# Kernel optimization log

Hardware: AMD Instinct MI355X
Metric: run time of the kernel (lower is better)

Reference implementation:

```python
import math
import jax, jax.numpy as jnp
import numpy as np

CAPACITY_FACTOR = 1.25  # _DEFAULT_EP_CAPACITY_FACTOR
STD = 0.02


def setup_inputs() -> dict:
    key = jax.random.key(0)
    k_x, k_r, k_ug, k_d = jax.random.split(key, 4)
    B, S, D, E, I = 8, 4096, 1024, 16, 2816
    x = jax.random.normal(k_x, (B, S, D), dtype=jnp.float32)
    router = STD * jax.random.truncated_normal(k_r, -3, 3, (D, E)).astype(jnp.float32)
    w_up_gate = STD * jax.random.truncated_normal(k_ug, -3, 3, (E, D, 2 * I)).astype(jnp.float32)
    w_down = STD * jax.random.truncated_normal(k_d, -3, 3, (E, I, D)).astype(jnp.float32)
    return {"x": x, "router": router, "w_up_gate": w_up_gate, "w_down": w_down,
            "num_experts_per_token": 2}


def _routing_stats(selected_experts, router_probs, router_logits, num_experts, k):
    probs = router_probs.astype(jnp.float32)
    logits = router_logits.astype(jnp.float32)
    expert_counts = jnp.sum(jax.nn.one_hot(selected_experts, num_experts, dtype=jnp.float32), axis=(0, 1))
    total = jnp.maximum(jnp.sum(expert_counts), 1.0)
    frac = expert_counts / total
    entropy = -jnp.sum(frac * jnp.log(frac + 1e-06))
    token_fraction = frac * k
    p = jnp.mean(probs, axis=0)
    lb_loss = num_experts * jnp.sum(token_fraction * p)
    z = jax.scipy.special.logsumexp(logits, axis=-1)
    z_loss = jnp.mean(z ** 2)
    return expert_counts, entropy, lb_loss, z_loss


def _moe_forward(x, router, w_up_gate, w_down, k):
    B, S, D = x.shape
    E = router.shape[1]
    T = B * S
    x_flat = x.reshape(T, D)

    router_logits = jnp.einsum('td,de->te', x_flat, router)          # [T,E]
    router_probs = jax.nn.softmax(router_logits, axis=-1)
    topk_logits, selected = jax.lax.top_k(router_logits, k)          # [T,K]
    combine = jax.nn.softmax(topk_logits, axis=-1).astype(x.dtype)   # [T,K]

    stats = _routing_stats(selected, router_probs, router_logits, E, k)

    # ---- capacity-based dispatch ----
    C = int(math.ceil(T * k / E * CAPACITY_FACTOR))                  # static
    TK = T * k
    flat_sel = selected.reshape(TK).astype(jnp.int32)                # token-major priority
    oh = jax.nn.one_hot(flat_sel, E, dtype=jnp.int32)                # [TK,E]
    pos = jnp.take_along_axis(jnp.cumsum(oh, axis=0), flat_sel[:, None], axis=1)[:, 0] - 1
    keep = pos < C                                                   # [TK]
    pos_safe = jnp.where(keep, pos, 0)
    token_idx = jnp.arange(TK, dtype=jnp.int32) // k

    vals = jnp.where(keep[:, None], x_flat[token_idx], 0.0)          # [TK,D]
    expert_in = jnp.zeros((E, C, D), dtype=x.dtype).at[flat_sel, pos_safe].add(vals)

    # ---- grouped SwiGLU MLP ----
    h = jnp.einsum('ecd,edf->ecf', expert_in, w_up_gate)             # [E,C,2I]
    I = w_down.shape[1]
    gate, up = h[..., :I], h[..., I:]
    act = jax.nn.silu(gate) * up                                     # [E,C,I]
    expert_out = jnp.einsum('eci,eid->ecd', act, w_down)             # [E,C,D]

    # ---- combine ----
    gathered = expert_out[flat_sel, pos_safe]                        # [TK,D]
    w = (combine.reshape(TK) * keep.astype(x.dtype))[:, None]
    routed = (gathered * w).reshape(T, k, D).sum(axis=1)             # [T,D]
    return routed.reshape(B, S, D), stats


def reference(x, router, w_up_gate, w_down, num_experts_per_token):
    routed, (counts, entropy, lb_loss, z_loss) = _moe_forward(
        x, router, w_up_gate, w_down, num_experts_per_token)
    return routed, counts, entropy, lb_loss, z_loss
```

## Files before the change

kernel.cpp:

```cpp
#include <hip/hip_runtime.h>
#include <math.h>

#define T_TOK 32768
#define TKA   65536
#define DIM   1024
#define NE    16
#define IDIM  2816
#define CAP   5120

typedef short short8 __attribute__((ext_vector_type(8)));
typedef float floatx4 __attribute__((ext_vector_type(4)));

__device__ __forceinline__ unsigned short f2bf(float f) {
  unsigned int u = __float_as_uint(f);
  u = u + 0x7FFFu + ((u >> 16) & 1u);
  return (unsigned short)(u >> 16);
}
__device__ __forceinline__ float bf2f(unsigned short h) {
  return __uint_as_float(((unsigned int)h) << 16);
}

__device__ __forceinline__ void gld_lds16(const void* g, void* l) {
  __builtin_amdgcn_global_load_lds(
      (const __attribute__((address_space(1))) unsigned int*)(unsigned long long)g,
      (__attribute__((address_space(3))) unsigned int*)(unsigned int)(unsigned long long)l,
      16, 0, 0);
}


__global__ void cvtx_kernel(const float* __restrict__ in, unsigned short* __restrict__ out) {
  size_t i = ((size_t)blockIdx.x * 256 + threadIdx.x) * 8;
  float4 a = *(const float4*)(in + i);
  float4 b = *(const float4*)(in + i + 4);
  short8 v;
  v[0] = (short)f2bf(a.x); v[1] = (short)f2bf(a.y); v[2] = (short)f2bf(a.z); v[3] = (short)f2bf(a.w);
  v[4] = (short)f2bf(b.x); v[5] = (short)f2bf(b.y); v[6] = (short)f2bf(b.z); v[7] = (short)f2bf(b.w);
  *(short8*)(out + i) = v;
}

__global__ void transpose_cvt(const float* __restrict__ in, unsigned short* __restrict__ out,
                              int R, int Cin) {
  int e = blockIdx.z;
  size_t base = (size_t)e * R * Cin;
  int ct = blockIdx.x;
  int rt = blockIdx.y;
  __shared__ unsigned short Ts[64][72];
  int tx = threadIdx.x & 63, ty = threadIdx.x >> 6;
#pragma unroll
  for (int j = 0; j < 16; j++) {
    int r = rt * 64 + ty + j * 4;
    int c = ct * 64 + tx;
    Ts[tx][ty + j * 4] = f2bf(in[base + (size_t)r * Cin + c]);
  }
  __syncthreads();
#pragma unroll
  for (int j = 0; j < 16; j++) {
    int cl = ty + j * 4;
    out[base + (size_t)(ct * 64 + cl) * R + rt * 64 + tx] = Ts[cl][tx];
  }
}


__global__ void router_kernel(const float* __restrict__ x, const float* __restrict__ router,
                              float* __restrict__ logits) {
  int tid = blockIdx.x * 256 + threadIdx.x;
  int tk = tid >> 4, e = tid & 15;
  const float* xr = x + (size_t)tk * DIM;
  float acc = 0.f;
#pragma unroll 8
  for (int d = 0; d < DIM; d++) acc = fmaf(xr[d], router[d * NE + e], acc);
  logits[tid] = acc;
}

__global__ void topk_kernel(const float* __restrict__ logits, int* __restrict__ sel,
                            float* __restrict__ wcomb, float* __restrict__ prob_sums,
                            int* __restrict__ counts_raw, float* __restrict__ z2sum) {
  __shared__ float ps[16];
  __shared__ int   cs[16];
  __shared__ float zs;
  int tid = threadIdx.x;
  if (tid < 16) { ps[tid] = 0.f; cs[tid] = 0; }
  if (tid == 0) zs = 0.f;
  __syncthreads();
  int t = blockIdx.x * 256 + tid;
  float l[16];
#pragma unroll
  for (int e = 0; e < 16; e++) l[e] = logits[(size_t)t * 16 + e];
  float m1 = l[0]; int e1 = 0;
#pragma unroll
  for (int e = 1; e < 16; e++) if (l[e] > m1) { m1 = l[e]; e1 = e; }
  float m2 = -3.4e38f; int e2 = 0;
#pragma unroll
  for (int e = 0; e < 16; e++) if (e != e1 && l[e] > m2) { m2 = l[e]; e2 = e; }
  float b  = __expf(m2 - m1);
  float w1 = 1.f / (1.f + b);
  sel[t * 2] = e1; sel[t * 2 + 1] = e2;
  wcomb[t * 2] = w1; wcomb[t * 2 + 1] = 1.f - w1;
  float s = 0.f;
  float pexp[16];
#pragma unroll
  for (int e = 0; e < 16; e++) { pexp[e] = __expf(l[e] - m1); s += pexp[e]; }
  float inv = 1.f / s;
#pragma unroll
  for (int e = 0; e < 16; e++) atomicAdd(&ps[e], pexp[e] * inv);
  atomicAdd(&cs[e1], 1); atomicAdd(&cs[e2], 1);
  float z = m1 + __logf(s);
  atomicAdd(&zs, z * z);
  __syncthreads();
  if (tid < 16) { atomicAdd(&prob_sums[tid], ps[tid]); atomicAdd(&counts_raw[tid], cs[tid]); }
  if (tid == 0) atomicAdd(z2sum, zs);
}

__global__ void hist_kernel(const int* __restrict__ sel, int* __restrict__ bhist) {
  __shared__ int h[16];
  int tid = threadIdx.x;
  if (tid < 16) h[tid] = 0;
  __syncthreads();
  atomicAdd(&h[sel[blockIdx.x * 256 + tid]], 1);
  __syncthreads();
  if (tid < 16) bhist[blockIdx.x * 16 + tid] = h[tid];
}

__global__ void scan_kernel(const int* __restrict__ bhist, int* __restrict__ bbase,
                            int* __restrict__ capc) {
  int e = threadIdx.x;
  if (e >= 16) return;
  int run = 0;
  for (int b = 0; b < 256; b++) { bbase[b * 16 + e] = run; run += bhist[b * 16 + e]; }
  capc[e] = run < CAP ? run : CAP;
}

__global__ void rank_kernel(const int* __restrict__ sel, const int* __restrict__ bbase,
                            int* __restrict__ pos_tk, int* __restrict__ scat) {
  __shared__ int se[256];
  int i = threadIdx.x;
  int a = blockIdx.x * 256 + i;
  int e = sel[a];
  se[i] = e;
  __syncthreads();
  int r = 0;
  for (int j = 0; j < i; j++) r += (se[j] == e) ? 1 : 0;
  int pos = bbase[blockIdx.x * 16 + e] + r;
  if (pos < CAP) { pos_tk[a] = pos; scat[e * CAP + pos] = a >> 1; }
  else           { pos_tk[a] = -1; }
}


__global__ __launch_bounds__(256) void gemm1_kernel(
    const unsigned short* __restrict__ xb, const unsigned short* __restrict__ wtg,
    const int* __restrict__ scat, const int* __restrict__ capc,
    const unsigned short* __restrict__ zrow, unsigned short* __restrict__ act) {
  int e = blockIdx.z, ct = blockIdx.x, it = blockIdx.y;
  if (ct * 128 >= capc[e]) return;
  __shared__ __align__(16) unsigned short As[128 * 64];
  __shared__ __align__(16) unsigned short Bg[64 * 64];
  __shared__ __align__(16) unsigned short Bu[64 * 64];
  const int t = threadIdx.x, w = t >> 6, l = t & 63;
  const int lr8   = l >> 3;
  const int koffs = ((l & 7) ^ lr8) * 8;

  const unsigned short* aptr[4];
#pragma unroll
  for (int j = 0; j < 4; j++) {
    int c0 = ct * 128 + w * 32 + j * 8 + lr8;
    int tok = scat[e * CAP + c0];
    aptr[j] = (tok >= 0 ? xb + (size_t)tok * DIM : zrow) + koffs;
  }
  const unsigned short* bgp[2];
  const unsigned short* bup[2];
#pragma unroll
  for (int j = 0; j < 2; j++) {
    int n0 = it * 64 + w * 16 + j * 8 + lr8;
    bgp[j] = wtg + ((size_t)e * (2 * IDIM) + n0) * DIM + koffs;
    bup[j] = bgp[j] + (size_t)IDIM * DIM;
  }

  floatx4 accg[8], accu[8];
#pragma unroll
  for (int i = 0; i < 8; i++) {
    accg[i] = (floatx4){0.f, 0.f, 0.f, 0.f};
    accu[i] = (floatx4){0.f, 0.f, 0.f, 0.f};
  }
  const int wm = w >> 1, wn = w & 1;
  const int rl = l & 15, lq = l >> 4, sx = l & 7;

  for (int k0 = 0; k0 < DIM; k0 += 64) {
    __syncthreads();
#pragma unroll
    for (int j = 0; j < 4; j++)
      gld_lds16(aptr[j] + k0, (char*)As + w * 4096 + j * 1024);
#pragma unroll
    for (int j = 0; j < 2; j++) {
      gld_lds16(bgp[j] + k0, (char*)Bg + w * 2048 + j * 1024);
      gld_lds16(bup[j] + k0, (char*)Bu + w * 2048 + j * 1024);
    }
    __syncthreads();
#pragma unroll
    for (int ks = 0; ks < 2; ks++) {
      const int slot = ((ks * 4 + lq) ^ sx) * 8;
      short8 af[4], bgf[2], buf2[2];
#pragma unroll
      for (int mi = 0; mi < 4; mi++)
        af[mi] = *(const short8*)(As + (wm * 64 + mi * 16 + rl) * 64 + slot);
#pragma unroll
      for (int ni = 0; ni < 2; ni++) {
        bgf[ni]  = *(const short8*)(Bg + (wn * 32 + ni * 16 + rl) * 64 + slot);
        buf2[ni] = *(const short8*)(Bu + (wn * 32 + ni * 16 + rl) * 64 + slot);
      }
#pragma unroll
      for (int mi = 0; mi < 4; mi++)
#pragma unroll
        for (int ni = 0; ni < 2; ni++) {
          accg[mi * 2 + ni] = __builtin_amdgcn_mfma_f32_16x16x32_bf16(af[mi], bgf[ni],  accg[mi * 2 + ni], 0, 0, 0);
          accu[mi * 2 + ni] = __builtin_amdgcn_mfma_f32_16x16x32_bf16(af[mi], buf2[ni], accu[mi * 2 + ni], 0, 0, 0);
        }
    }
  }

  size_t abase = ((size_t)e * CAP + (size_t)ct * 128) * IDIM + (size_t)it * 64;
#pragma unroll
  for (int mi = 0; mi < 4; mi++)
#pragma unroll
    for (int reg = 0; reg < 4; reg++) {
      int m = wm * 64 + mi * 16 + lq * 4 + reg;
#pragma unroll
      for (int ni = 0; ni < 2; ni++) {
        int n = wn * 32 + ni * 16 + (l & 15);
        float g = accg[mi * 2 + ni][reg];
        float u = accu[mi * 2 + ni][reg];
        float a = g / (1.f + __expf(-g)) * u;
        act[abase + (size_t)m * IDIM + n] = f2bf(a);
      }
    }
}


__global__ __launch_bounds__(256) void gemm2_kernel(
    const unsigned short* __restrict__ act, const unsigned short* __restrict__ wtd,
    const int* __restrict__ capc, unsigned short* __restrict__ eout) {
  int e = blockIdx.z, ct = blockIdx.x, it = blockIdx.y;
  if (ct * 128 >= capc[e]) return;
  __shared__ __align__(16) unsigned short As[128 * 64];
  __shared__ __align__(16) unsigned short Bs[64 * 64];
  const int t = threadIdx.x, w = t >> 6, l = t & 63;
  const int lr8   = l >> 3;
  const int koffs = ((l & 7) ^ lr8) * 8;

  const unsigned short* aptr[4];
#pragma unroll
  for (int j = 0; j < 4; j++)
    aptr[j] = act + ((size_t)e * CAP + ct * 128 + w * 32 + j * 8 + lr8) * IDIM + koffs;
  const unsigned short* bptr[2];
#pragma unroll
  for (int j = 0; j < 2; j++)
    bptr[j] = wtd + ((size_t)e * DIM + it * 64 + w * 16 + j * 8 + lr8) * IDIM + koffs;

  floatx4 acc[8];
#pragma unroll
  for (int i = 0; i < 8; i++) acc[i] = (floatx4){0.f, 0.f, 0.f, 0.f};
  const int wm = w >> 1, wn = w & 1;
  const int rl = l & 15, lq = l >> 4, sx = l & 7;

  for (int k0 = 0; k0 < IDIM; k0 += 64) {
    __syncthreads();
#pragma unroll
    for (int j = 0; j < 4; j++)
      gld_lds16(aptr[j] + k0, (char*)As + w * 4096 + j * 1024);
#pragma unroll
    for (int j = 0; j < 2; j++)
      gld_lds16(bptr[j] + k0, (char*)Bs + w * 2048 + j * 1024);
    __syncthreads();
#pragma unroll
    for (int ks = 0; ks < 2; ks++) {
      const int slot = ((ks * 4 + lq) ^ sx) * 8;
      short8 af[4], bf2[2];
#pragma unroll
      for (int mi = 0; mi < 4; mi++)
        af[mi] = *(const short8*)(As + (wm * 64 + mi * 16 + rl) * 64 + slot);
#pragma unroll
      for (int ni = 0; ni < 2; ni++)
        bf2[ni] = *(const short8*)(Bs + (wn * 32 + ni * 16 + rl) * 64 + slot);
#pragma unroll
      for (int mi = 0; mi < 4; mi++)
#pragma unroll
        for (int ni = 0; ni < 2; ni++)
          acc[mi * 2 + ni] = __builtin_amdgcn_mfma_f32_16x16x32_bf16(af[mi], bf2[ni], acc[mi * 2 + ni], 0, 0, 0);
    }
  }

  size_t obase = ((size_t)e * CAP + (size_t)ct * 128) * DIM + (size_t)it * 64;
#pragma unroll
  for (int mi = 0; mi < 4; mi++)
#pragma unroll
    for (int reg = 0; reg < 4; reg++) {
      int m = wm * 64 + mi * 16 + lq * 4 + reg;
#pragma unroll
      for (int ni = 0; ni < 2; ni++) {
        int n = wn * 32 + ni * 16 + (l & 15);
        eout[obase + (size_t)m * DIM + n] = f2bf(acc[mi * 2 + ni][reg]);
      }
    }
}


__global__ void combine_kernel(const unsigned short* __restrict__ eout,
                               const int* __restrict__ sel, const int* __restrict__ pos_tk,
                               const float* __restrict__ wcomb, float* __restrict__ routed) {
  int tok = blockIdx.x;
  int d = threadIdx.x * 4;
  float a0 = 0.f, a1 = 0.f, a2 = 0.f, a3 = 0.f;
#pragma unroll
  for (int s = 0; s < 2; s++) {
    int a = tok * 2 + s;
    int p = pos_tk[a];
    if (p >= 0) {
      int e = sel[a];
      float wgt = wcomb[a];
      const unsigned short* row = eout + ((size_t)e * CAP + p) * DIM + d;
      ushort4 r = *(const ushort4*)row;
      a0 += wgt * bf2f(r.x); a1 += wgt * bf2f(r.y);
      a2 += wgt * bf2f(r.z); a3 += wgt * bf2f(r.w);
    }
  }
  float4 o = {a0, a1, a2, a3};
  *(float4*)(routed + (size_t)tok * DIM + d) = o;
}

__global__ void finalize_kernel(const int* __restrict__ counts_raw, const float* __restrict__ psums,
                                const float* __restrict__ z2sum, float* __restrict__ tail) {
  if (threadIdx.x != 0 || blockIdx.x != 0) return;
  float ent = 0.f, lb = 0.f;
  for (int e = 0; e < 16; e++) {
    float c = (float)counts_raw[e];
    tail[e] = c;
    float frac = c / 65536.f;
    ent -= frac * logf(frac + 1e-6f);
    lb += frac * 2.f * (psums[e] / 32768.f);
  }
  tail[16] = ent;
  tail[17] = 16.f * lb;
  tail[18] = z2sum[0] / 32768.f;
}


extern "C" void kernel_launch(void* const* d_in, const int* in_sizes, int n_in,
                              void* d_out, int out_size, void* d_ws, size_t ws_size,
                              hipStream_t stream) {
  (void)in_sizes; (void)n_in; (void)out_size; (void)ws_size;
  const float* x         = (const float*)d_in[0];
  const float* router    = (const float*)d_in[1];
  const float* w_up_gate = (const float*)d_in[2];
  const float* w_down    = (const float*)d_in[3];
  float* out = (float*)d_out;

  char* p = (char*)d_ws;
  size_t off = 0;
  auto alc = [&](size_t n) { void* r = p + off; off += (n + 255) & ~(size_t)255; return r; };

  unsigned short* xb   = (unsigned short*)alc((size_t)T_TOK * DIM * 2);
  unsigned short* wtg  = (unsigned short*)alc((size_t)NE * 2 * IDIM * DIM * 2);
  unsigned short* wtd  = (unsigned short*)alc((size_t)NE * DIM * IDIM * 2);
  unsigned short* act  = (unsigned short*)alc((size_t)NE * CAP * IDIM * 2);
  unsigned short* eout = (unsigned short*)alc((size_t)NE * CAP * DIM * 2);
  float* logits = (float*)alc((size_t)T_TOK * NE * 4);
  int*   sel    = (int*)alc((size_t)TKA * 4);
  float* wcomb  = (float*)alc((size_t)TKA * 4);
  int*   pos_tk = (int*)alc((size_t)TKA * 4);
  int*   scat   = (int*)alc((size_t)NE * CAP * 4);
  int*   bhist  = (int*)alc(256 * 16 * 4);
  int*   bbase  = (int*)alc(256 * 16 * 4);
  int*   capc   = (int*)alc(64);
  int*   counts_raw = (int*)alc(64);
  float* psums  = (float*)alc(64);
  float* z2     = (float*)alc(64);
  unsigned short* zrow = (unsigned short*)alc(DIM * 2);

  hipMemsetAsync(counts_raw, 0, 64, stream);
  hipMemsetAsync(psums, 0, 64, stream);
  hipMemsetAsync(z2, 0, 64, stream);
  hipMemsetAsync(scat, 0xFF, (size_t)NE * CAP * 4, stream);
  hipMemsetAsync(zrow, 0, DIM * 2, stream);

  cvtx_kernel<<<T_TOK * DIM / (256 * 8), 256, 0, stream>>>(x, xb);
  transpose_cvt<<<dim3(2 * IDIM / 64, DIM / 64, NE), 256, 0, stream>>>(w_up_gate, wtg, DIM, 2 * IDIM);
  transpose_cvt<<<dim3(DIM / 64, IDIM / 64, NE), 256, 0, stream>>>(w_down, wtd, IDIM, DIM);

  router_kernel<<<T_TOK * NE / 256, 256, 0, stream>>>(x, router, logits);
  topk_kernel<<<T_TOK / 256, 256, 0, stream>>>(logits, sel, wcomb, psums, counts_raw, z2);
  hist_kernel<<<TKA / 256, 256, 0, stream>>>(sel, bhist);
  scan_kernel<<<1, 64, 0, stream>>>(bhist, bbase, capc);
  rank_kernel<<<TKA / 256, 256, 0, stream>>>(sel, bbase, pos_tk, scat);

  gemm1_kernel<<<dim3(CAP / 128, IDIM / 64, NE), 256, 0, stream>>>(xb, wtg, scat, capc, zrow, act);
  gemm2_kernel<<<dim3(CAP / 128, DIM / 64, NE), 256, 0, stream>>>(act, wtd, capc, eout);

  combine_kernel<<<T_TOK, 256, 0, stream>>>(eout, sel, pos_tk, wcomb, out);
  finalize_kernel<<<1, 64, 0, stream>>>(counts_raw, psums, z2, out + (size_t)T_TOK * DIM);
}
```

Measured before the change: 2.482 ms.

## Double-buffer LDS tiles in both expert GEMMs and stage scan input in LDS

Both grouped GEMM kernels now keep two LDS buffers for the A and B tiles. Each iteration issues the asynchronous global-to-LDS loads for the next K slice before running the MFMAs on the current one, and uses one barrier per stage instead of two. The goal is to hide global load latency behind matrix math. In exchange, LDS use per block doubles (about 64KB for gemm1 and 48KB for gemm2), which can cut the number of resident blocks per CU. The scan kernel also copies the block histogram into shared memory with all 256 threads before the 16-thread serial prefix scan.

```diff
diff --git a/kernel.cpp b/kernel.cpp
--- a/kernel.cpp
+++ b/kernel.cpp
@@ -123,11 +123,16 @@
 
 __global__ void scan_kernel(const int* __restrict__ bhist, int* __restrict__ bbase,
                             int* __restrict__ capc) {
-  int e = threadIdx.x;
-  if (e >= 16) return;
-  int run = 0;
-  for (int b = 0; b < 256; b++) { bbase[b * 16 + e] = run; run += bhist[b * 16 + e]; }
-  capc[e] = run < CAP ? run : CAP;
+  __shared__ int h[256 * 16];
+  int t = threadIdx.x;
+  for (int i = t; i < 256 * 16 / 4; i += 256)
+    ((int4*)h)[i] = ((const int4*)bhist)[i];
+  __syncthreads();
+  if (t < 16) {
+    int run = 0;
+    for (int b = 0; b < 256; b++) { bbase[b * 16 + t] = run; run += h[b * 16 + t]; }
+    capc[t] = run < CAP ? run : CAP;
+  }
 }
 
 __global__ void rank_kernel(const int* __restrict__ sel, const int* __restrict__ bbase,
@@ -152,9 +157,9 @@
     const unsigned short* __restrict__ zrow, unsigned short* __restrict__ act) {
   int e = blockIdx.z, ct = blockIdx.x, it = blockIdx.y;
   if (ct * 128 >= capc[e]) return;
-  __shared__ __align__(16) unsigned short As[128 * 64];
-  __shared__ __align__(16) unsigned short Bg[64 * 64];
-  __shared__ __align__(16) unsigned short Bu[64 * 64];
+  __shared__ __align__(16) unsigned short As0[128 * 64], As1[128 * 64];
+  __shared__ __align__(16) unsigned short Bg0[64 * 64],  Bg1[64 * 64];
+  __shared__ __align__(16) unsigned short Bu0[64 * 64],  Bu1[64 * 64];
   const int t = threadIdx.x, w = t >> 6, l = t & 63;
   const int lr8   = l >> 3;
   const int koffs = ((l & 7) ^ lr8) * 8;
@@ -184,8 +189,7 @@
   const int wm = w >> 1, wn = w & 1;
   const int rl = l & 15, lq = l >> 4, sx = l & 7;
 
-  for (int k0 = 0; k0 < DIM; k0 += 64) {
-    __syncthreads();
+  auto stage = [&](int k0, unsigned short* As, unsigned short* Bg, unsigned short* Bu) {
 #pragma unroll
     for (int j = 0; j < 4; j++)
       gld_lds16(aptr[j] + k0, (char*)As + w * 4096 + j * 1024);
@@ -194,7 +198,9 @@
       gld_lds16(bgp[j] + k0, (char*)Bg + w * 2048 + j * 1024);
       gld_lds16(bup[j] + k0, (char*)Bu + w * 2048 + j * 1024);
     }
-    __syncthreads();
+  };
+  auto compute = [&](const unsigned short* As, const unsigned short* Bg,
+                     const unsigned short* Bu) {
 #pragma unroll
     for (int ks = 0; ks < 2; ks++) {
       const int slot = ((ks * 4 + lq) ^ sx) * 8;
@@ -215,6 +221,17 @@
           accu[mi * 2 + ni] = __builtin_amdgcn_mfma_f32_16x16x32_bf16(af[mi], buf2[ni], accu[mi * 2 + ni], 0, 0, 0);
         }
     }
+  };
+
+  stage(0, As0, Bg0, Bu0);
+  __syncthreads();
+  for (int k0 = 0; k0 < DIM; k0 += 128) {
+    stage(k0 + 64, As1, Bg1, Bu1);
+    compute(As0, Bg0, Bu0);
+    __syncthreads();
+    if (k0 + 128 < DIM) stage(k0 + 128, As0, Bg0, Bu0);
+    compute(As1, Bg1, Bu1);
+    __syncthreads();
   }
 
   size_t abase = ((size_t)e * CAP + (size_t)ct * 128) * IDIM + (size_t)it * 64;
@@ -240,8 +257,8 @@
     const int* __restrict__ capc, unsigned short* __restrict__ eout) {
   int e = blockIdx.z, ct = blockIdx.x, it = blockIdx.y;
   if (ct * 128 >= capc[e]) return;
-  __shared__ __align__(16) unsigned short As[128 * 64];
-  __shared__ __align__(16) unsigned short Bs[64 * 64];
+  __shared__ __align__(16) unsigned short As0[128 * 64], As1[128 * 64];
+  __shared__ __align__(16) unsigned short Bs0[64 * 64],  Bs1[64 * 64];
   const int t = threadIdx.x, w = t >> 6, l = t & 63;
   const int lr8   = l >> 3;
   const int koffs = ((l & 7) ^ lr8) * 8;
@@ -261,15 +278,15 @@
   const int wm = w >> 1, wn = w & 1;
   const int rl = l & 15, lq = l >> 4, sx = l & 7;
 
-  for (int k0 = 0; k0 < IDIM; k0 += 64) {
-    __syncthreads();
+  auto stage = [&](int k0, unsigned short* As, unsigned short* Bs) {
 #pragma unroll
     for (int j = 0; j < 4; j++)
       gld_lds16(aptr[j] + k0, (char*)As + w * 4096 + j * 1024);
 #pragma unroll
     for (int j = 0; j < 2; j++)
       gld_lds16(bptr[j] + k0, (char*)Bs + w * 2048 + j * 1024);
-    __syncthreads();
+  };
+  auto compute = [&](const unsigned short* As, const unsigned short* Bs) {
 #pragma unroll
     for (int ks = 0; ks < 2; ks++) {
       const int slot = ((ks * 4 + lq) ^ sx) * 8;
@@ -286,6 +303,17 @@
         for (int ni = 0; ni < 2; ni++)
           acc[mi * 2 + ni] = __builtin_amdgcn_mfma_f32_16x16x32_bf16(af[mi], bf2[ni], acc[mi * 2 + ni], 0, 0, 0);
     }
+  };
+
+  stage(0, As0, Bs0);
+  __syncthreads();
+  for (int k0 = 0; k0 < IDIM; k0 += 128) {
+    stage(k0 + 64, As1, Bs1);
+    compute(As0, Bs0);
+    __syncthreads();
+    if (k0 + 128 < IDIM) stage(k0 + 128, As0, Bs0);
+    compute(As1, Bs1);
+    __syncthreads();
   }
 
   size_t obase = ((size_t)e * CAP + (size_t)ct * 128) * DIM + (size_t)it * 64;
@@ -388,7 +416,7 @@
   router_kernel<<<T_TOK * NE / 256, 256, 0, stream>>>(x, router, logits);
   topk_kernel<<<T_TOK / 256, 256, 0, stream>>>(logits, sel, wcomb, psums, counts_raw, z2);
   hist_kernel<<<TKA / 256, 256, 0, stream>>>(sel, bhist);
-  scan_kernel<<<1, 64, 0, stream>>>(bhist, bbase, capc);
+  scan_kernel<<<1, 256, 0, stream>>>(bhist, bbase, capc);
   rank_kernel<<<TKA / 256, 256, 0, stream>>>(sel, bbase, pos_tk, scat);
 
   gemm1_kernel<<<dim3(CAP / 128, IDIM / 64, NE), 256, 0, stream>>>(xb, wtg, scat, capc, zrow, act);
```

Result: faster. 2.351 ms (-5.3%).
